# Performance work log

Hardware: AMD Instinct MI355X
Metric: run time of the kernel (lower is better)

## Reference

```python
import jax, jax.numpy as jnp
import numpy as np

B, U1, U2 = 4, 2048, 2048
C = 256      # in_feat_dim
F = 256      # feat_dim
M = 4        # num_modes
D = C // M   # attention_mode_dim = 64
ATTN_CLIP = 500.0
LN_EPS = 1e-12


def setup_inputs() -> dict:
    key = jax.random.key(0)
    ks = jax.random.split(key, 8)
    s = 0.02  # base_initializer_range
    inp = {
        "query_feat": jax.random.normal(ks[0], (B, U1, C), jnp.float32),
        "key_feat": jax.random.normal(ks[1], (B, U2, C), jnp.float32),
        "Wq": jax.random.normal(ks[2], (M * D, C), jnp.float32) * s,
        "bq": jnp.zeros((M * D,), jnp.float32),
    }
    # tie_qk_scheme='shared': key linear shares query weights
    inp["Wk"] = inp["Wq"]
    inp["bk"] = inp["bq"]
    inp["Wv"] = jax.random.normal(ks[3], (M * F, C), jnp.float32) * s  # first_linear, v_has_bias=False
    inp["W_mid"] = jax.random.normal(ks[4], (F, F), jnp.float32) * s   # MMSharedMid shared_linear
    inp["b_mid"] = jnp.zeros((F,), jnp.float32)
    inp["W_out"] = jax.random.normal(ks[5], (M, F, F), jnp.float32) * s  # grouped 1x1 conv, per mode
    inp["b_out"] = jnp.zeros((M, F), jnp.float32)
    inp["ln_g"] = jnp.ones((F,), jnp.float32)   # resout LayerNorm
    inp["ln_b"] = jnp.zeros((F,), jnp.float32)
    inp["W_score"] = jax.random.normal(ks[6], (1, F), jnp.float32) * s  # LearnedSoftAggregate
    inp["b_score"] = jnp.zeros((1,), jnp.float32)
    return inp


def _layer_norm(x, g, b):
    mu = jnp.mean(x, axis=-1, keepdims=True)
    var = jnp.var(x, axis=-1, keepdims=True)
    return (x - mu) * jax.lax.rsqrt(var + LN_EPS) * g + b


def reference(query_feat, key_feat, Wq, bq, Wk, bk, Wv, W_mid, b_mid,
              W_out, b_out, ln_g, ln_b, W_score, b_score):
    # --- tied-QK multi-mode attention ---
    q = (query_feat @ Wq.T + bq).reshape(B, U1, M, D)
    k = (key_feat @ Wk.T + bk).reshape(B, U2, M, D)
    scores = jnp.einsum('bimd,bjmd->bmij', q, k) / jnp.sqrt(jnp.float32(D))
    scores = jnp.clip(scores, -ATTN_CLIP, ATTN_CLIP)  # attn_clip
    probs = jax.nn.softmax(scores, axis=-1)           # [B, M, U1, U2]

    # --- ExpandedFeatTrans: value projection + fusion ---
    v = (key_feat @ Wv.T).reshape(B, U2, M, F)        # first_linear (no bias)
    fused = jnp.einsum('bmij,bjmf->bmif', probs, v)   # [B, M, U1, F]

    # MMSharedMid: shared linear over F + gelu (dropout = identity in eval)
    mid = jax.nn.gelu(fused @ W_mid.T + b_mid, approximate=False)

    # MMPrivateOutput: per-mode grouped 1x1 conv; NOTE the original code computes
    # x_comb = x + shortcut but then layer-norms x (shortcut dropped) - kept faithful.
    out = jnp.einsum('bmif,mgf->bmig', mid, W_out) + b_out[None, :, None, :]
    out = _layer_norm(out, ln_g, ln_b)                # [B, M, U1, F]

    # LearnedSoftAggregate over modes (group_dim=1, keepdim=False)
    mode_scores = out @ W_score.T + b_score           # [B, M, U1, 1]
    mode_probs = jax.nn.softmax(mode_scores, axis=1)
    return jnp.sum(out * mode_probs, axis=1)          # [B, U1, F]
```

## Files before the change

### kernel.cpp

```cpp
#include <hip/hip_runtime.h>

typedef __attribute__((ext_vector_type(8))) short short8;
typedef __attribute__((ext_vector_type(4))) float f32x4;
typedef __attribute__((ext_vector_type(16))) float f32x16;
typedef unsigned short u16t;
typedef unsigned int u32t;

#define MFMA16(a, b, c) __builtin_amdgcn_mfma_f32_16x16x32_bf16((a), (b), (c), 0, 0, 0)
#define MFMA32(a, b, c) __builtin_amdgcn_mfma_f32_32x32x16_bf16((a), (b), (c), 0, 0, 0)

__device__ __forceinline__ u16t f2bf(float f) {
  u32t u = __float_as_uint(f);
  u32t r = u + 0x7fffu + ((u >> 16) & 1u);
  return (u16t)(r >> 16);
}
__device__ __forceinline__ float bf2f(u16t b) {
  return __uint_as_float(((u32t)b) << 16);
}
__device__ __forceinline__ short8 pack8(float4 a0, float4 a1) {
  short8 r;
  r[0] = (short)f2bf(a0.x); r[1] = (short)f2bf(a0.y);
  r[2] = (short)f2bf(a0.z); r[3] = (short)f2bf(a0.w);
  r[4] = (short)f2bf(a1.x); r[5] = (short)f2bf(a1.y);
  r[6] = (short)f2bf(a1.z); r[7] = (short)f2bf(a1.w);
  return r;
}
__device__ __forceinline__ u32t packrhu(float a, float b) {
  u32t ua = __float_as_uint(a) + 0x8000u;
  u32t ub = __float_as_uint(b) + 0x8000u;
  return (ua >> 16) | (ub & 0xffff0000u);
}

__global__ __launch_bounds__(256) void cvt_kernel(
    const float* __restrict__ Wq, const float* __restrict__ Wv,
    const float* __restrict__ Wm, const float* __restrict__ Wo,
    u16t* __restrict__ WqB, u16t* __restrict__ WvB,
    u16t* __restrict__ WmB, u16t* __restrict__ WoB) {
  const int blk = blockIdx.x, tid = threadIdx.x;
  const float* src; u16t* dst; int base;
  if (blk < 64)       { src = Wq; dst = WqB; base = blk * 1024; }
  else if (blk < 320) { src = Wv; dst = WvB; base = (blk - 64) * 1024; }
  else if (blk < 384) { src = Wm; dst = WmB; base = (blk - 320) * 1024; }
  else                { src = Wo; dst = WoB; base = (blk - 384) * 1024; }
  int i = base + tid * 4;
  float4 v = *(const float4*)(src + i);
  ushort4 o;
  o.x = f2bf(v.x); o.y = f2bf(v.y); o.z = f2bf(v.z); o.w = f2bf(v.w);
  *(ushort4*)(dst + i) = o;
}

__global__ __launch_bounds__(256) void proj_kernel(
    const float* __restrict__ query, const float* __restrict__ key,
    const u16t* __restrict__ WqB, const u16t* __restrict__ WvB,
    const float* __restrict__ bq,
    u16t* __restrict__ QfB, u16t* __restrict__ KfB, u16t* __restrict__ VfB) {
  __shared__ __align__(16) u16t As[64 * 264];
  __shared__ __align__(16) u16t Ws[2][64 * 72];

  const int blk = blockIdx.x;
  const int tid = threadIdx.x;
  const int w = tid >> 6, lane = tid & 63, quad = lane >> 4, l15 = lane & 15;
  const int l31 = lane & 31, h8 = (lane >> 5) * 8;
  const int wrow = (w >> 1) * 32, wcol = (w & 1) * 32;
  const int r2 = tid >> 3, c8 = tid & 7;

  const float* A; const u16t* W16; const float* bias;
  float scale; u16t* outp; int mode, bx, by0;
  if (blk < 128) {
    A = query; W16 = WqB; bias = bq; scale = 0.125f; outp = QfB; mode = 0; bx = blk; by0 = 0;
  } else if (blk < 256) {
    A = key; W16 = WqB; bias = bq; scale = 1.0f; outp = KfB; mode = 0; bx = blk - 128; by0 = 0;
  } else {
    int v2 = blk - 256;
    A = key; W16 = WvB; bias = nullptr; scale = 1.0f; outp = VfB; mode = 1;
    bx = v2 & 127; by0 = (v2 >> 7) * 4;
  }
  const int rt = bx * 64;

#pragma unroll
  for (int hh = 0; hh < 2; ++hh) {
    int rr = r2 + hh * 32;
    const float* arow = A + (size_t)(rt + rr) * 256;
#pragma unroll
    for (int kt = 0; kt < 4; ++kt) {
      const float4* pa = (const float4*)(arow + kt * 64 + c8 * 8);
      float4 a0 = pa[0], a1 = pa[1];
      a0.x *= scale; a0.y *= scale; a0.z *= scale; a0.w *= scale;
      a1.x *= scale; a1.y *= scale; a1.z *= scale; a1.w *= scale;
      *(short8*)&As[rr * 264 + kt * 64 + c8 * 8] = pack8(a0, a1);
    }
  }
  __syncthreads();

  short8 af[8][2];
#pragma unroll
  for (int ks8 = 0; ks8 < 8; ++ks8) {
    af[ks8][0] = *(const short8*)&As[(wrow + l15) * 264 + ks8 * 32 + quad * 8];
    af[ks8][1] = *(const short8*)&As[(wrow + 16 + l15) * 264 + ks8 * 32 + quad * 8];
  }

#pragma unroll
  for (int hh = 0; hh < 2; ++hh) {
    int rr = r2 + hh * 32;
    *(short8*)&Ws[0][rr * 72 + c8 * 8] =
        *(const short8*)(W16 + (size_t)(by0 * 64 + rr) * 256 + c8 * 8);
  }
  __syncthreads();

  const f32x4 fz = {0.f, 0.f, 0.f, 0.f};
  f32x4 acc[2][2];
#pragma unroll
  for (int i = 0; i < 2; i++)
#pragma unroll
    for (int j = 0; j < 2; j++) acc[i][j] = fz;

#pragma unroll 1
  for (int nt = 0; nt < 4; ++nt) {
    const int by = by0 + nt;
    const int ct = by * 64;

#pragma unroll
    for (int kt = 0; kt < 4; ++kt) {
      short8 wst[2];
      const bool havenext = (nt < 3) || (kt < 3);
      if (havenext) {
        const int ctn = (kt < 3) ? ct : (ct + 64);
        const int ktn = (kt + 1) & 3;
#pragma unroll
        for (int hh = 0; hh < 2; ++hh) {
          int rr = r2 + hh * 32;
          wst[hh] = *(const short8*)(W16 + (size_t)(ctn + rr) * 256 + ktn * 64 + c8 * 8);
        }
      }
      const u16t* Wb = &Ws[kt & 1][0];
#pragma unroll
      for (int ks = 0; ks < 2; ++ks) {
        short8 bw0 = *(const short8*)&Wb[(wcol + l15) * 72 + ks * 32 + quad * 8];
        short8 bw1 = *(const short8*)&Wb[(wcol + 16 + l15) * 72 + ks * 32 + quad * 8];
        acc[0][0] = MFMA16(af[kt * 2 + ks][0], bw0, acc[0][0]);
        acc[0][1] = MFMA16(af[kt * 2 + ks][0], bw1, acc[0][1]);
        acc[1][0] = MFMA16(af[kt * 2 + ks][1], bw0, acc[1][0]);
        acc[1][1] = MFMA16(af[kt * 2 + ks][1], bw1, acc[1][1]);
      }
      if (havenext) {
#pragma unroll
        for (int hh = 0; hh < 2; ++hh) {
          int rr = r2 + hh * 32;
          *(short8*)&Ws[(kt + 1) & 1][rr * 72 + c8 * 8] = wst[hh];
        }
      }
      __syncthreads();
    }

    u16t* Cs = As;
    if (mode == 0) {
#pragma unroll
      for (int i = 0; i < 2; i++) {
        int rl = wrow + i * 16 + quad * 4;
#pragma unroll
        for (int j = 0; j < 2; j++) {
          int cl = wcol + j * 16 + l15;
          float bv = bias ? bias[ct + cl] * scale : 0.f;
#pragma unroll
          for (int rg = 0; rg < 4; ++rg)
            Cs[(rl + rg) * 72 + cl] = f2bf(acc[i][j][rg] + bv);
        }
      }
    } else {
#pragma unroll
      for (int i = 0; i < 2; i++) {
        int rl = wrow + i * 16 + quad * 4;
#pragma unroll
        for (int j = 0; j < 2; j++) {
          int cl = wcol + j * 16 + l15;
          ushort4 pk;
          pk.x = f2bf(acc[i][j][0]);
          pk.y = f2bf(acc[i][j][1]);
          pk.z = f2bf(acc[i][j][2]);
          pk.w = f2bf(acc[i][j][3]);
          *(ushort4*)&Cs[cl * 72 + rl] = pk;
        }
      }
    }
    __syncthreads();
#pragma unroll
    for (int t2 = 0; t2 < 2; ++t2) {
      short8 frag = *(const short8*)&Cs[(t2 * 32 + l31) * 72 + w * 16 + h8];
      size_t base;
      if (mode == 0) {
        int b = rt >> 11, m = by;
        int it32 = ((rt & 2047) >> 5) + t2;
        base = (((size_t)(b * 4 + m) * 64 + it32) * 4 + w) * 512;
      } else {
        int b = rt >> 11, m = by >> 2;
        int fb = ((by & 3) << 1) + t2;
        int jt16 = ((rt & 2047) >> 4) + w;
        base = (((size_t)(b * 4 + m) * 8 + fb) * 128 + jt16) * 512;
      }
      *(short8*)(outp + base + lane * 8) = frag;
    }
#pragma unroll
    for (int i = 0; i < 2; i++)
#pragma unroll
      for (int j = 0; j < 2; j++) acc[i][j] = fz;
  }
}

__global__ __launch_bounds__(256, 4) void attn_kernel(
    const u16t* __restrict__ Qf, const u16t* __restrict__ Kf,
    const u16t* __restrict__ Vf,
    const u16t* __restrict__ Wmid, const u16t* __restrict__ Wout,
    const float* __restrict__ b_mid, const float* __restrict__ b_out,
    const float* __restrict__ ln_g, const float* __restrict__ ln_b,
    const float* __restrict__ Wsc, const float* __restrict__ b_sc,
    u16t* __restrict__ out_ln, float* __restrict__ scoresWS) {
  __shared__ __align__(16) u16t smU[8448];
  __shared__ float smL[128];
  __shared__ float smR[128];
  __shared__ float smS[64];
  const int tid = threadIdx.x;
  const int w = tid >> 6, lane = tid & 63, quad = lane >> 4, l15 = lane & 15;
  const int l31 = lane & 31, h = lane >> 5;
  const int L = blockIdx.x;
  const int xcd = L & 7, slot = L >> 3;
  const int bm = xcd * 2 + (slot >> 6);
  const int it32 = slot & 63;
  const int m = bm & 3;
  const int q0 = it32 * 32;

  const size_t lane8 = (size_t)lane * 8;

  const u16t* qbase = Qf + ((size_t)(bm * 64 + it32) * 4) * 512 + lane8;
  short8 qf4[4];
#pragma unroll
  for (int ksd = 0; ksd < 4; ++ksd)
    qf4[ksd] = *(const short8*)(qbase + ksd * 512);

  const u16t* kbase = Kf + ((size_t)bm * 256) * 512 + lane8;
  const u16t* vbase = Vf + ((size_t)(bm * 8 + 2 * w) * 128) * 512 + lane8;

  f32x16 facc[2];
#pragma unroll
  for (int j = 0; j < 2; j++)
#pragma unroll
    for (int r = 0; r < 16; r++) facc[j][r] = 0.f;
  float lsum = 0.f;

  short8 kf4[4];
#pragma unroll
  for (int ksd = 0; ksd < 4; ++ksd)
    kf4[ksd] = *(const short8*)(kbase + (size_t)w * 2048 + ksd * 512);

  {
    f32x16 sacc;
#pragma unroll
    for (int r = 0; r < 16; r++) sacc[r] = 0.f;
#pragma unroll
    for (int ksd = 0; ksd < 4; ++ksd)
      sacc = MFMA32(kf4[ksd], qf4[ksd], sacc);
    float ls = 0.f;
#pragma unroll
    for (int tt = 0; tt < 8; ++tt) {
      const int jl = ((2 * tt) & 3) + 8 * ((2 * tt) >> 2) + 4 * h;
      float p0 = __expf(sacc[2 * tt]);
      float p1 = __expf(sacc[2 * tt + 1]);
      ls += p0 + p1;
      *(u32t*)&smU[l31 * 132 + w * 32 + jl] = packrhu(p0, p1);
    }
    lsum += ls;
  }
#pragma unroll
  for (int ksd = 0; ksd < 4; ++ksd)
    kf4[ksd] = *(const short8*)(kbase + (size_t)(4 + w) * 2048 + ksd * 512);
  __syncthreads();

#pragma unroll 1
  for (int t = 0; t < 16; ++t) {
    u16t* Pb = (t & 1) ? smU + 4224 : smU;
    u16t* Pn = (t & 1) ? smU : smU + 4224;

    if (t < 15) {
      f32x16 sacc;
#pragma unroll
      for (int r = 0; r < 16; r++) sacc[r] = 0.f;
#pragma unroll
      for (int ksd = 0; ksd < 4; ++ksd)
        sacc = MFMA32(kf4[ksd], qf4[ksd], sacc);
      float ls = 0.f;
#pragma unroll
      for (int tt = 0; tt < 8; ++tt) {
        const int jl = ((2 * tt) & 3) + 8 * ((2 * tt) >> 2) + 4 * h;
        float p0 = __expf(sacc[2 * tt]);
        float p1 = __expf(sacc[2 * tt + 1]);
        ls += p0 + p1;
        *(u32t*)&Pn[l31 * 132 + w * 32 + jl] = packrhu(p0, p1);
      }
      lsum += ls;
    }
    if (t < 14) {
      const int jn = (t + 2) * 4 + w;
#pragma unroll
      for (int ksd = 0; ksd < 4; ++ksd)
        kf4[ksd] = *(const short8*)(kbase + (size_t)jn * 2048 + ksd * 512);
    }
#pragma unroll
    for (int jj = 0; jj < 4; ++jj) {
      short8 vf[2][2];
#pragma unroll
      for (int fb = 0; fb < 2; ++fb)
#pragma unroll
        for (int ks2 = 0; ks2 < 2; ++ks2)
          vf[fb][ks2] = *(const short8*)(vbase + ((size_t)fb * 128 + (t * 8 + jj * 2 + ks2)) * 512);
      short8 bbL[2];
#pragma unroll
      for (int ks2 = 0; ks2 < 2; ++ks2)
        bbL[ks2] = *(const short8*)&Pb[l31 * 132 + jj * 32 + ks2 * 16 + h * 8];
      facc[0] = MFMA32(vf[0][0], bbL[0], facc[0]);
      facc[0] = MFMA32(vf[0][1], bbL[1], facc[0]);
      facc[1] = MFMA32(vf[1][0], bbL[0], facc[1]);
      facc[1] = MFMA32(vf[1][1], bbL[1], facc[1]);
    }
    __syncthreads();
  }

  lsum += __shfl_xor(lsum, 32);
  if (h == 0) smL[w * 32 + l31] = lsum;
  __syncthreads();
  float inv = 1.f / (smL[l31] + smL[32 + l31] + smL[64 + l31] + smL[96 + l31]);

  u16t* const smF = smU;
#pragma unroll
  for (int fb = 0; fb < 2; ++fb) {
#pragma unroll
    for (int g = 0; g < 4; ++g) {
      int fbase = w * 64 + fb * 32 + 8 * g + 4 * h;
      ushort4 pk4;
      pk4.x = f2bf(facc[fb][4 * g + 0] * inv);
      pk4.y = f2bf(facc[fb][4 * g + 1] * inv);
      pk4.z = f2bf(facc[fb][4 * g + 2] * inv);
      pk4.w = f2bf(facc[fb][4 * g + 3] * inv);
      *(ushort4*)&smF[l31 * 264 + fbase] = pk4;
    }
  }
  __syncthreads();

  const int rgrp = w >> 1, ch = w & 1;
  const int rowq = rgrp * 16 + quad * 4;
  const f32x4 fz4 = {0.f, 0.f, 0.f, 0.f};

  f32x4 macc[8];
#pragma unroll
  for (int i = 0; i < 8; i++) macc[i] = fz4;
  for (int kc = 0; kc < 8; ++kc) {
    short8 af = *(const short8*)&smF[(rgrp * 16 + l15) * 264 + kc * 32 + quad * 8];
#pragma unroll
    for (int nb = 0; nb < 8; ++nb) {
      short8 bw = *(const short8*)(Wmid + (size_t)(ch * 128 + nb * 16 + l15) * 256 + kc * 32 + quad * 8);
      macc[nb] = MFMA16(af, bw, macc[nb]);
    }
  }
#pragma unroll
  for (int nb = 0; nb < 8; ++nb) {
    int c = ch * 128 + nb * 16 + l15;
    float bmv = b_mid[c];
#pragma unroll
    for (int rg = 0; rg < 4; ++rg) {
      float x = macc[nb][rg] + bmv;
      macc[nb][rg] = 0.5f * x * (1.f + erff(x * 0.70710678118654752f));
    }
  }
  __syncthreads();
#pragma unroll
  for (int nb = 0; nb < 8; ++nb)
#pragma unroll
    for (int rg = 0; rg < 4; ++rg)
      smF[(rowq + rg) * 264 + ch * 128 + nb * 16 + l15] = f2bf(macc[nb][rg]);
  __syncthreads();

  const u16t* Wo = Wout + (size_t)m * 65536;
  f32x4 oacc[8];
#pragma unroll
  for (int i = 0; i < 8; i++) oacc[i] = fz4;
  for (int kc = 0; kc < 8; ++kc) {
    short8 af = *(const short8*)&smF[(rgrp * 16 + l15) * 264 + kc * 32 + quad * 8];
#pragma unroll
    for (int nb = 0; nb < 8; ++nb) {
      short8 bw = *(const short8*)(Wo + (size_t)(ch * 128 + nb * 16 + l15) * 256 + kc * 32 + quad * 8);
      oacc[nb] = MFMA16(af, bw, oacc[nb]);
    }
  }

  float sum[4] = {0, 0, 0, 0}, sq[4] = {0, 0, 0, 0};
#pragma unroll
  for (int nb = 0; nb < 8; ++nb) {
    int c = ch * 128 + nb * 16 + l15;
    float bo = b_out[m * 256 + c];
#pragma unroll
    for (int rg = 0; rg < 4; ++rg) {
      float x = oacc[nb][rg] + bo;
      oacc[nb][rg] = x;
      sum[rg] += x;
      sq[rg] += x * x;
    }
  }
#pragma unroll
  for (int rg = 0; rg < 4; ++rg) {
    float s = sum[rg], s2 = sq[rg];
    s += __shfl_xor(s, 1); s += __shfl_xor(s, 2); s += __shfl_xor(s, 4); s += __shfl_xor(s, 8);
    s2 += __shfl_xor(s2, 1); s2 += __shfl_xor(s2, 2); s2 += __shfl_xor(s2, 4); s2 += __shfl_xor(s2, 8);
    if (l15 == 0) {
      smR[(rowq + rg) + 32 * ch] = s;
      smR[64 + (rowq + rg) + 32 * ch] = s2;
    }
  }
  __syncthreads();
  float mu[4], rstd[4];
#pragma unroll
  for (int rg = 0; rg < 4; ++rg) {
    int r = rowq + rg;
    float s = smR[r] + smR[r + 32];
    float s2 = smR[64 + r] + smR[64 + r + 32];
    float mean = s * (1.f / 256.f);
    float var = s2 * (1.f / 256.f) - mean * mean;
    mu[rg] = mean;
    rstd[rg] = rsqrtf(var + 1e-12f);
  }

  float scp[4] = {0, 0, 0, 0};
#pragma unroll
  for (int nb = 0; nb < 8; ++nb) {
    int c = ch * 128 + nb * 16 + l15;
    float g = ln_g[c], bb2 = ln_b[c], wsv = Wsc[c];
#pragma unroll
    for (int rg = 0; rg < 4; ++rg) {
      float xn = (oacc[nb][rg] - mu[rg]) * rstd[rg] * g + bb2;
      out_ln[((size_t)bm * 2048 + (q0 + rowq + rg)) * 256 + c] = f2bf(xn);
      scp[rg] += xn * wsv;
    }
  }
#pragma unroll
  for (int rg = 0; rg < 4; ++rg) {
    float s = scp[rg];
    s += __shfl_xor(s, 1); s += __shfl_xor(s, 2); s += __shfl_xor(s, 4); s += __shfl_xor(s, 8);
    if (l15 == 0) smS[(rowq + rg) + 32 * ch] = s;
  }
  __syncthreads();
  if (ch == 0 && l15 == 0) {
#pragma unroll
    for (int rg = 0; rg < 4; ++rg) {
      int r = rowq + rg;
      scoresWS[bm * 2048 + q0 + r] = smS[r] + smS[r + 32] + b_sc[0];
    }
  }
}

__global__ __launch_bounds__(256) void agg_kernel(
    const u16t* __restrict__ out_ln, const float* __restrict__ scoresWS,
    float* __restrict__ out) {
  const int row = blockIdx.x;
  const int c = threadIdx.x;
  const int b = row >> 11, i = row & 2047;
  float s0 = scoresWS[(b * 4 + 0) * 2048 + i];
  float s1 = scoresWS[(b * 4 + 1) * 2048 + i];
  float s2 = scoresWS[(b * 4 + 2) * 2048 + i];
  float s3 = scoresWS[(b * 4 + 3) * 2048 + i];
  float mx = fmaxf(fmaxf(s0, s1), fmaxf(s2, s3));
  float e0 = __expf(s0 - mx), e1 = __expf(s1 - mx), e2 = __expf(s2 - mx), e3 = __expf(s3 - mx);
  float inv = 1.f / (e0 + e1 + e2 + e3);
  float acc = e0 * inv * bf2f(out_ln[((size_t)(b * 4 + 0) * 2048 + i) * 256 + c]) +
              e1 * inv * bf2f(out_ln[((size_t)(b * 4 + 1) * 2048 + i) * 256 + c]) +
              e2 * inv * bf2f(out_ln[((size_t)(b * 4 + 2) * 2048 + i) * 256 + c]) +
              e3 * inv * bf2f(out_ln[((size_t)(b * 4 + 3) * 2048 + i) * 256 + c]);
  out[(size_t)row * 256 + c] = acc;
}

extern "C" void kernel_launch(void* const* d_in, const int* in_sizes, int n_in,
                              void* d_out, int out_size, void* d_ws, size_t ws_size,
                              hipStream_t stream) {
  (void)in_sizes; (void)n_in; (void)out_size; (void)ws_size;
  const float* query = (const float*)d_in[0];
  const float* key   = (const float*)d_in[1];
  const float* Wq    = (const float*)d_in[2];
  const float* bq    = (const float*)d_in[3];
  const float* Wv    = (const float*)d_in[6];
  const float* Wm    = (const float*)d_in[7];
  const float* bmid  = (const float*)d_in[8];
  const float* Wo    = (const float*)d_in[9];
  const float* bo    = (const float*)d_in[10];
  const float* lng   = (const float*)d_in[11];
  const float* lnb   = (const float*)d_in[12];
  const float* Wsc   = (const float*)d_in[13];
  const float* bsc   = (const float*)d_in[14];

  char* p = (char*)d_ws;
  u16t* QfB = (u16t*)p; p += (size_t)2097152 * 2;
  u16t* KfB = (u16t*)p; p += (size_t)2097152 * 2;
  u16t* VfB = (u16t*)p; p += (size_t)8388608 * 2;
  u16t* WmB = (u16t*)p; p += (size_t)65536 * 2;
  u16t* WoB = (u16t*)p; p += (size_t)262144 * 2;
  u16t* WqB = (u16t*)p; p += (size_t)65536 * 2;
  u16t* WvB = (u16t*)p; p += (size_t)262144 * 2;
  u16t* outLn = (u16t*)p; p += (size_t)8388608 * 2;
  float* scWS = (float*)p; p += (size_t)32768 * 4;

  cvt_kernel<<<640, 256, 0, stream>>>(Wq, Wv, Wm, Wo, WqB, WvB, WmB, WoB);

  proj_kernel<<<768, 256, 0, stream>>>(query, key, WqB, WvB, bq,
                                       QfB, KfB, VfB);

  attn_kernel<<<1024, 256, 0, stream>>>(QfB, KfB, VfB, WmB, WoB,
                                        bmid, bo, lng, lnb, Wsc, bsc,
                                        outLn, scWS);

  agg_kernel<<<8192, 256, 0, stream>>>(outLn, scWS, (float*)d_out);
}
```

Before: 235.0 us.

## Split attention over key halves with atomic fp32 accumulation and separate combine kernel

```diff
diff --git a/kernel.cpp b/kernel.cpp
--- a/kernel.cpp
+++ b/kernel.cpp
@@ -35,8 +35,23 @@
     const float* __restrict__ Wq, const float* __restrict__ Wv,
     const float* __restrict__ Wm, const float* __restrict__ Wo,
     u16t* __restrict__ WqB, u16t* __restrict__ WvB,
-    u16t* __restrict__ WmB, u16t* __restrict__ WoB) {
+    u16t* __restrict__ WmB, u16t* __restrict__ WoB,
+    float* __restrict__ Facc, float* __restrict__ Lsum) {
   const int blk = blockIdx.x, tid = threadIdx.x;
+  if (blk >= 1152) {
+    float* dst = Lsum + (blk - 1152) * 16384 + tid * 4;
+    const float4 z = {0.f, 0.f, 0.f, 0.f};
+#pragma unroll
+    for (int k = 0; k < 16; ++k) *(float4*)(dst + k * 1024) = z;
+    return;
+  }
+  if (blk >= 640) {
+    float* dst = Facc + (size_t)(blk - 640) * 16384 + tid * 4;
+    const float4 z = {0.f, 0.f, 0.f, 0.f};
+#pragma unroll
+    for (int k = 0; k < 16; ++k) *(float4*)(dst + k * 1024) = z;
+    return;
+  }
   const float* src; u16t* dst; int base;
   if (blk < 64)       { src = Wq; dst = WqB; base = blk * 1024; }
   else if (blk < 320) { src = Wv; dst = WvB; base = (blk - 64) * 1024; }
@@ -203,6 +218,290 @@
     for (int i = 0; i < 2; i++)
 #pragma unroll
       for (int j = 0; j < 2; j++) acc[i][j] = fz;
+  }
+}
+
+__global__ __launch_bounds__(256, 4) void attn_part_kernel(
+    const u16t* __restrict__ Qf, const u16t* __restrict__ Kf,
+    const u16t* __restrict__ Vf,
+    float* __restrict__ Facc, float* __restrict__ Lsum) {
+  __shared__ __align__(16) u16t smU[8448];
+  __shared__ float smL[128];
+  const int tid = threadIdx.x;
+  const int w = tid >> 6, lane = tid & 63, l15 = lane & 15;
+  const int l31 = lane & 31, h = lane >> 5;
+  (void)l15;
+  const int L = blockIdx.x;
+  const int xcd = L & 7, slot = L >> 3;
+  const int bm = xcd * 2 + (slot >> 7);
+  const int rest = slot & 127;
+  const int it32 = rest >> 1;
+  const int half = rest & 1;
+  const int t0 = half * 8;
+
+  const size_t lane8 = (size_t)lane * 8;
+
+  const u16t* qbase = Qf + ((size_t)(bm * 64 + it32) * 4) * 512 + lane8;
+  short8 qf4[4];
+#pragma unroll
+  for (int ksd = 0; ksd < 4; ++ksd)
+    qf4[ksd] = *(const short8*)(qbase + ksd * 512);
+
+  const u16t* kbase = Kf + ((size_t)bm * 256) * 512 + lane8;
+  const u16t* vbase = Vf + ((size_t)(bm * 8 + 2 * w) * 128) * 512 + lane8;
+
+  f32x16 facc[2];
+#pragma unroll
+  for (int j = 0; j < 2; j++)
+#pragma unroll
+    for (int r = 0; r < 16; r++) facc[j][r] = 0.f;
+  float lsum = 0.f;
+
+  short8 kf4[4];
+#pragma unroll
+  for (int ksd = 0; ksd < 4; ++ksd)
+    kf4[ksd] = *(const short8*)(kbase + (size_t)(t0 * 4 + w) * 2048 + ksd * 512);
+
+  {
+    f32x16 sacc;
+#pragma unroll
+    for (int r = 0; r < 16; r++) sacc[r] = 0.f;
+#pragma unroll
+    for (int ksd = 0; ksd < 4; ++ksd)
+      sacc = MFMA32(kf4[ksd], qf4[ksd], sacc);
+    float ls = 0.f;
+#pragma unroll
+    for (int tt = 0; tt < 8; ++tt) {
+      const int jl = ((2 * tt) & 3) + 8 * ((2 * tt) >> 2) + 4 * h;
+      float p0 = __expf(sacc[2 * tt]);
+      float p1 = __expf(sacc[2 * tt + 1]);
+      ls += p0 + p1;
+      *(u32t*)&smU[l31 * 132 + w * 32 + jl] = packrhu(p0, p1);
+    }
+    lsum += ls;
+  }
+#pragma unroll
+  for (int ksd = 0; ksd < 4; ++ksd)
+    kf4[ksd] = *(const short8*)(kbase + (size_t)((t0 + 1) * 4 + w) * 2048 + ksd * 512);
+  __syncthreads();
+
+#pragma unroll 1
+  for (int tl = 0; tl < 8; ++tl) {
+    const int t = t0 + tl;
+    u16t* Pb = (tl & 1) ? smU + 4224 : smU;
+    u16t* Pn = (tl & 1) ? smU : smU + 4224;
+
+    if (tl < 7) {
+      f32x16 sacc;
+#pragma unroll
+      for (int r = 0; r < 16; r++) sacc[r] = 0.f;
+#pragma unroll
+      for (int ksd = 0; ksd < 4; ++ksd)
+        sacc = MFMA32(kf4[ksd], qf4[ksd], sacc);
+      float ls = 0.f;
+#pragma unroll
+      for (int tt = 0; tt < 8; ++tt) {
+        const int jl = ((2 * tt) & 3) + 8 * ((2 * tt) >> 2) + 4 * h;
+        float p0 = __expf(sacc[2 * tt]);
+        float p1 = __expf(sacc[2 * tt + 1]);
+        ls += p0 + p1;
+        *(u32t*)&Pn[l31 * 132 + w * 32 + jl] = packrhu(p0, p1);
+      }
+      lsum += ls;
+    }
+    if (tl < 6) {
+      const int jn = (t + 2) * 4 + w;
+#pragma unroll
+      for (int ksd = 0; ksd < 4; ++ksd)
+        kf4[ksd] = *(const short8*)(kbase + (size_t)jn * 2048 + ksd * 512);
+    }
+#pragma unroll
+    for (int jj = 0; jj < 4; ++jj) {
+      short8 vf[2][2];
+#pragma unroll
+      for (int fb = 0; fb < 2; ++fb)
+#pragma unroll
+        for (int ks2 = 0; ks2 < 2; ++ks2)
+          vf[fb][ks2] = *(const short8*)(vbase + ((size_t)fb * 128 + (t * 8 + jj * 2 + ks2)) * 512);
+      short8 bbL[2];
+#pragma unroll
+      for (int ks2 = 0; ks2 < 2; ++ks2)
+        bbL[ks2] = *(const short8*)&Pb[l31 * 132 + jj * 32 + ks2 * 16 + h * 8];
+      facc[0] = MFMA32(vf[0][0], bbL[0], facc[0]);
+      facc[0] = MFMA32(vf[0][1], bbL[1], facc[0]);
+      facc[1] = MFMA32(vf[1][0], bbL[0], facc[1]);
+      facc[1] = MFMA32(vf[1][1], bbL[1], facc[1]);
+    }
+    __syncthreads();
+  }
+
+  lsum += __shfl_xor(lsum, 32);
+  if (h == 0) smL[w * 32 + l31] = lsum;
+  __syncthreads();
+  const size_t tbase = ((size_t)(bm * 64 + it32)) * 32;
+  if (tid < 32) {
+    float lh = smL[tid] + smL[32 + tid] + smL[64 + tid] + smL[96 + tid];
+    atomicAdd(&Lsum[tbase + tid], lh);
+  }
+  float* Fb = Facc + (tbase + l31) * 256;
+#pragma unroll
+  for (int fb = 0; fb < 2; ++fb)
+#pragma unroll
+    for (int g = 0; g < 4; ++g)
+#pragma unroll
+      for (int e = 0; e < 4; ++e) {
+        int f = w * 64 + fb * 32 + 8 * g + 4 * h + e;
+        atomicAdd(&Fb[f], facc[fb][4 * g + e]);
+      }
+}
+
+__global__ __launch_bounds__(256, 4) void combine_kernel(
+    const float* __restrict__ Facc, const float* __restrict__ Lsum,
+    const u16t* __restrict__ Wmid, const u16t* __restrict__ Wout,
+    const float* __restrict__ b_mid, const float* __restrict__ b_out,
+    const float* __restrict__ ln_g, const float* __restrict__ ln_b,
+    const float* __restrict__ Wsc, const float* __restrict__ b_sc,
+    u16t* __restrict__ out_ln, float* __restrict__ scoresWS) {
+  __shared__ __align__(16) u16t smF[8448];
+  __shared__ float smR[128];
+  __shared__ float smS[64];
+  __shared__ float smLi[32];
+  const int tid = threadIdx.x;
+  const int w = tid >> 6, lane = tid & 63, quad = lane >> 4, l15 = lane & 15;
+  const int L = blockIdx.x;
+  const int xcd = L & 7, slot = L >> 3;
+  const int bm = xcd * 2 + (slot >> 6);
+  const int it32 = slot & 63;
+  const int m = bm & 3;
+  const int q0 = it32 * 32;
+
+  const size_t tbase = ((size_t)(bm * 64 + it32)) * 32;
+  if (tid < 32) smLi[tid] = 1.f / Lsum[tbase + tid];
+  __syncthreads();
+
+  const float* Fsrc = Facc + tbase * 256;
+#pragma unroll
+  for (int k = 0; k < 8; ++k) {
+    int flat = (k * 256 + tid) * 4;
+    int row = flat >> 8, f = flat & 255;
+    float4 v = *(const float4*)(Fsrc + flat);
+    float inv = smLi[row];
+    ushort4 pk4;
+    pk4.x = f2bf(v.x * inv);
+    pk4.y = f2bf(v.y * inv);
+    pk4.z = f2bf(v.z * inv);
+    pk4.w = f2bf(v.w * inv);
+    *(ushort4*)&smF[row * 264 + f] = pk4;
+  }
+  __syncthreads();
+
+  const int rgrp = w >> 1, ch = w & 1;
+  const int rowq = rgrp * 16 + quad * 4;
+  const f32x4 fz4 = {0.f, 0.f, 0.f, 0.f};
+
+  f32x4 macc[8];
+#pragma unroll
+  for (int i = 0; i < 8; i++) macc[i] = fz4;
+  for (int kc = 0; kc < 8; ++kc) {
+    short8 af = *(const short8*)&smF[(rgrp * 16 + l15) * 264 + kc * 32 + quad * 8];
+#pragma unroll
+    for (int nb = 0; nb < 8; ++nb) {
+      short8 bw = *(const short8*)(Wmid + (size_t)(ch * 128 + nb * 16 + l15) * 256 + kc * 32 + quad * 8);
+      macc[nb] = MFMA16(af, bw, macc[nb]);
+    }
+  }
+#pragma unroll
+  for (int nb = 0; nb < 8; ++nb) {
+    int c = ch * 128 + nb * 16 + l15;
+    float bmv = b_mid[c];
+#pragma unroll
+    for (int rg = 0; rg < 4; ++rg) {
+      float x = macc[nb][rg] + bmv;
+      macc[nb][rg] = 0.5f * x * (1.f + erff(x * 0.70710678118654752f));
+    }
+  }
+  __syncthreads();
+#pragma unroll
+  for (int nb = 0; nb < 8; ++nb)
+#pragma unroll
+    for (int rg = 0; rg < 4; ++rg)
+      smF[(rowq + rg) * 264 + ch * 128 + nb * 16 + l15] = f2bf(macc[nb][rg]);
+  __syncthreads();
+
+  const u16t* Wo = Wout + (size_t)m * 65536;
+  f32x4 oacc[8];
+#pragma unroll
+  for (int i = 0; i < 8; i++) oacc[i] = fz4;
+  for (int kc = 0; kc < 8; ++kc) {
+    short8 af = *(const short8*)&smF[(rgrp * 16 + l15) * 264 + kc * 32 + quad * 8];
+#pragma unroll
+    for (int nb = 0; nb < 8; ++nb) {
+      short8 bw = *(const short8*)(Wo + (size_t)(ch * 128 + nb * 16 + l15) * 256 + kc * 32 + quad * 8);
+      oacc[nb] = MFMA16(af, bw, oacc[nb]);
+    }
+  }
+
+  float sum[4] = {0, 0, 0, 0}, sq[4] = {0, 0, 0, 0};
+#pragma unroll
+  for (int nb = 0; nb < 8; ++nb) {
+    int c = ch * 128 + nb * 16 + l15;
+    float bo = b_out[m * 256 + c];
+#pragma unroll
+    for (int rg = 0; rg < 4; ++rg) {
+      float x = oacc[nb][rg] + bo;
+      oacc[nb][rg] = x;
+      sum[rg] += x;
+      sq[rg] += x * x;
+    }
+  }
+#pragma unroll
+  for (int rg = 0; rg < 4; ++rg) {
+    float s = sum[rg], s2 = sq[rg];
+    s += __shfl_xor(s, 1); s += __shfl_xor(s, 2); s += __shfl_xor(s, 4); s += __shfl_xor(s, 8);
+    s2 += __shfl_xor(s2, 1); s2 += __shfl_xor(s2, 2); s2 += __shfl_xor(s2, 4); s2 += __shfl_xor(s2, 8);
+    if (l15 == 0) {
+      smR[(rowq + rg) + 32 * ch] = s;
+      smR[64 + (rowq + rg) + 32 * ch] = s2;
+    }
+  }
+  __syncthreads();
+  float mu[4], rstd[4];
+#pragma unroll
+  for (int rg = 0; rg < 4; ++rg) {
+    int r = rowq + rg;
+    float s = smR[r] + smR[r + 32];
+    float s2 = smR[64 + r] + smR[64 + r + 32];
+    float mean = s * (1.f / 256.f);
+    float var = s2 * (1.f / 256.f) - mean * mean;
+    mu[rg] = mean;
+    rstd[rg] = rsqrtf(var + 1e-12f);
+  }
+
+  float scp[4] = {0, 0, 0, 0};
+#pragma unroll
+  for (int nb = 0; nb < 8; ++nb) {
+    int c = ch * 128 + nb * 16 + l15;
+    float g = ln_g[c], bb2 = ln_b[c], wsv = Wsc[c];
+#pragma unroll
+    for (int rg = 0; rg < 4; ++rg) {
+      float xn = (oacc[nb][rg] - mu[rg]) * rstd[rg] * g + bb2;
+      out_ln[((size_t)bm * 2048 + (q0 + rowq + rg)) * 256 + c] = f2bf(xn);
+      scp[rg] += xn * wsv;
+    }
+  }
+#pragma unroll
+  for (int rg = 0; rg < 4; ++rg) {
+    float s = scp[rg];
+    s += __shfl_xor(s, 1); s += __shfl_xor(s, 2); s += __shfl_xor(s, 4); s += __shfl_xor(s, 8);
+    if (l15 == 0) smS[(rowq + rg) + 32 * ch] = s;
+  }
+  __syncthreads();
+  if (ch == 0 && l15 == 0) {
+#pragma unroll
+    for (int rg = 0; rg < 4; ++rg) {
+      int r = rowq + rg;
+      scoresWS[bm * 2048 + q0 + r] = smS[r] + smS[r + 32] + b_sc[0];
+    }
   }
 }
 
@@ -477,7 +776,7 @@
 extern "C" void kernel_launch(void* const* d_in, const int* in_sizes, int n_in,
                               void* d_out, int out_size, void* d_ws, size_t ws_size,
                               hipStream_t stream) {
-  (void)in_sizes; (void)n_in; (void)out_size; (void)ws_size;
+  (void)in_sizes; (void)n_in; (void)out_size;
   const float* query = (const float*)d_in[0];
   const float* key   = (const float*)d_in[1];
   const float* Wq    = (const float*)d_in[2];
@@ -500,17 +799,34 @@
   u16t* WoB = (u16t*)p; p += (size_t)262144 * 2;
   u16t* WqB = (u16t*)p; p += (size_t)65536 * 2;
   u16t* WvB = (u16t*)p; p += (size_t)262144 * 2;
-  u16t* outLn = (u16t*)p; p += (size_t)8388608 * 2;
-  float* scWS = (float*)p; p += (size_t)32768 * 4;
-
-  cvt_kernel<<<640, 256, 0, stream>>>(Wq, Wv, Wm, Wo, WqB, WvB, WmB, WoB);
-
-  proj_kernel<<<768, 256, 0, stream>>>(query, key, WqB, WvB, bq,
-                                       QfB, KfB, VfB);
-
-  attn_kernel<<<1024, 256, 0, stream>>>(QfB, KfB, VfB, WmB, WoB,
-                                        bmid, bo, lng, lnb, Wsc, bsc,
-                                        outLn, scWS);
-
-  agg_kernel<<<8192, 256, 0, stream>>>(outLn, scWS, (float*)d_out);
-}
+  float* Facc = (float*)p;
+  float* Lsum = (float*)(p + (size_t)33554432);
+  float* scWS_s = (float*)(p + (size_t)33554432 + 131072);
+  const size_t need_split = ((char*)scWS_s - (char*)d_ws) + 131072;
+  u16t* outLn_s = (u16t*)d_ws;
+
+  const bool use_split = ws_size >= need_split;
+
+  if (use_split) {
+    cvt_kernel<<<1154, 256, 0, stream>>>(Wq, Wv, Wm, Wo, WqB, WvB, WmB, WoB,
+                                         Facc, Lsum);
+    proj_kernel<<<768, 256, 0, stream>>>(query, key, WqB, WvB, bq,
+                                         QfB, KfB, VfB);
+    attn_part_kernel<<<2048, 256, 0, stream>>>(QfB, KfB, VfB, Facc, Lsum);
+    combine_kernel<<<1024, 256, 0, stream>>>(Facc, Lsum, WmB, WoB,
+                                             bmid, bo, lng, lnb, Wsc, bsc,
+                                             outLn_s, scWS_s);
+    agg_kernel<<<8192, 256, 0, stream>>>(outLn_s, scWS_s, (float*)d_out);
+  } else {
+    u16t* outLn = (u16t*)p; p += (size_t)8388608 * 2;
+    float* scWS = (float*)p; p += (size_t)32768 * 4;
+    cvt_kernel<<<640, 256, 0, stream>>>(Wq, Wv, Wm, Wo, WqB, WvB, WmB, WoB,
+                                        nullptr, nullptr);
+    proj_kernel<<<768, 256, 0, stream>>>(query, key, WqB, WvB, bq,
+                                         QfB, KfB, VfB);
+    attn_kernel<<<1024, 256, 0, stream>>>(QfB, KfB, VfB, WmB, WoB,
+                                          bmid, bo, lng, lnb, Wsc, bsc,
+                                          outLn, scWS);
+    agg_kernel<<<8192, 256, 0, stream>>>(outLn, scWS, (float*)d_out);
+  }
+}
```

Measured after the change: 627.9 us. 167% more time.

## Deepen P-tile shared-memory pipeline to four buffers, one barrier per two tiles

Applied to the files above, without the earlier changes.

```diff
diff --git a/kernel.cpp b/kernel.cpp
--- a/kernel.cpp
+++ b/kernel.cpp
@@ -214,7 +214,7 @@
     const float* __restrict__ ln_g, const float* __restrict__ ln_b,
     const float* __restrict__ Wsc, const float* __restrict__ b_sc,
     u16t* __restrict__ out_ln, float* __restrict__ scoresWS) {
-  __shared__ __align__(16) u16t smU[8448];
+  __shared__ __align__(16) u16t smU[16896];
   __shared__ float smL[128];
   __shared__ float smR[128];
   __shared__ float smS[64];
@@ -251,57 +251,58 @@
   for (int ksd = 0; ksd < 4; ++ksd)
     kf4[ksd] = *(const short8*)(kbase + (size_t)w * 2048 + ksd * 512);
 
-  {
+#pragma unroll
+  for (int pt = 0; pt < 2; ++pt) {
     f32x16 sacc;
 #pragma unroll
     for (int r = 0; r < 16; r++) sacc[r] = 0.f;
 #pragma unroll
     for (int ksd = 0; ksd < 4; ++ksd)
       sacc = MFMA32(kf4[ksd], qf4[ksd], sacc);
+#pragma unroll
+    for (int ksd = 0; ksd < 4; ++ksd)
+      kf4[ksd] = *(const short8*)(kbase + (size_t)((pt + 1) * 4 + w) * 2048 + ksd * 512);
     float ls = 0.f;
+    u16t* Pw = smU + pt * 4224;
 #pragma unroll
     for (int tt = 0; tt < 8; ++tt) {
       const int jl = ((2 * tt) & 3) + 8 * ((2 * tt) >> 2) + 4 * h;
       float p0 = __expf(sacc[2 * tt]);
       float p1 = __expf(sacc[2 * tt + 1]);
       ls += p0 + p1;
-      *(u32t*)&smU[l31 * 132 + w * 32 + jl] = packrhu(p0, p1);
+      *(u32t*)&Pw[l31 * 132 + w * 32 + jl] = packrhu(p0, p1);
     }
     lsum += ls;
   }
-#pragma unroll
-  for (int ksd = 0; ksd < 4; ++ksd)
-    kf4[ksd] = *(const short8*)(kbase + (size_t)(4 + w) * 2048 + ksd * 512);
   __syncthreads();
 
 #pragma unroll 1
-  for (int t = 0; t < 16; ++t) {
-    u16t* Pb = (t & 1) ? smU + 4224 : smU;
-    u16t* Pn = (t & 1) ? smU : smU + 4224;
-
-    if (t < 15) {
+  for (int p = 0; p < 8; ++p) {
+    const int t0 = 2 * p;
+    u16t* Pb0 = smU + ((t0) & 3) * 4224;
+    u16t* Pb1 = smU + ((t0 + 1) & 3) * 4224;
+
+    if (p < 7) {
       f32x16 sacc;
 #pragma unroll
       for (int r = 0; r < 16; r++) sacc[r] = 0.f;
 #pragma unroll
       for (int ksd = 0; ksd < 4; ++ksd)
         sacc = MFMA32(kf4[ksd], qf4[ksd], sacc);
+#pragma unroll
+      for (int ksd = 0; ksd < 4; ++ksd)
+        kf4[ksd] = *(const short8*)(kbase + (size_t)((t0 + 3) * 4 + w) * 2048 + ksd * 512);
       float ls = 0.f;
+      u16t* Pn0 = smU + ((t0 + 2) & 3) * 4224;
 #pragma unroll
       for (int tt = 0; tt < 8; ++tt) {
         const int jl = ((2 * tt) & 3) + 8 * ((2 * tt) >> 2) + 4 * h;
         float p0 = __expf(sacc[2 * tt]);
         float p1 = __expf(sacc[2 * tt + 1]);
         ls += p0 + p1;
-        *(u32t*)&Pn[l31 * 132 + w * 32 + jl] = packrhu(p0, p1);
+        *(u32t*)&Pn0[l31 * 132 + w * 32 + jl] = packrhu(p0, p1);
       }
       lsum += ls;
-    }
-    if (t < 14) {
-      const int jn = (t + 2) * 4 + w;
-#pragma unroll
-      for (int ksd = 0; ksd < 4; ++ksd)
-        kf4[ksd] = *(const short8*)(kbase + (size_t)jn * 2048 + ksd * 512);
     }
 #pragma unroll
     for (int jj = 0; jj < 4; ++jj) {
@@ -310,11 +311,52 @@
       for (int fb = 0; fb < 2; ++fb)
 #pragma unroll
         for (int ks2 = 0; ks2 < 2; ++ks2)
-          vf[fb][ks2] = *(const short8*)(vbase + ((size_t)fb * 128 + (t * 8 + jj * 2 + ks2)) * 512);
+          vf[fb][ks2] = *(const short8*)(vbase + ((size_t)fb * 128 + (t0 * 8 + jj * 2 + ks2)) * 512);
       short8 bbL[2];
 #pragma unroll
       for (int ks2 = 0; ks2 < 2; ++ks2)
-        bbL[ks2] = *(const short8*)&Pb[l31 * 132 + jj * 32 + ks2 * 16 + h * 8];
+        bbL[ks2] = *(const short8*)&Pb0[l31 * 132 + jj * 32 + ks2 * 16 + h * 8];
+      facc[0] = MFMA32(vf[0][0], bbL[0], facc[0]);
+      facc[0] = MFMA32(vf[0][1], bbL[1], facc[0]);
+      facc[1] = MFMA32(vf[1][0], bbL[0], facc[1]);
+      facc[1] = MFMA32(vf[1][1], bbL[1], facc[1]);
+    }
+    if (p < 7) {
+      f32x16 sacc;
+#pragma unroll
+      for (int r = 0; r < 16; r++) sacc[r] = 0.f;
+#pragma unroll
+      for (int ksd = 0; ksd < 4; ++ksd)
+        sacc = MFMA32(kf4[ksd], qf4[ksd], sacc);
+      if (p < 6) {
+#pragma unroll
+        for (int ksd = 0; ksd < 4; ++ksd)
+          kf4[ksd] = *(const short8*)(kbase + (size_t)((t0 + 4) * 4 + w) * 2048 + ksd * 512);
+      }
+      float ls = 0.f;
+      u16t* Pn1 = smU + ((t0 + 3) & 3) * 4224;
+#pragma unroll
+      for (int tt = 0; tt < 8; ++tt) {
+        const int jl = ((2 * tt) & 3) + 8 * ((2 * tt) >> 2) + 4 * h;
+        float p0 = __expf(sacc[2 * tt]);
+        float p1 = __expf(sacc[2 * tt + 1]);
+        ls += p0 + p1;
+        *(u32t*)&Pn1[l31 * 132 + w * 32 + jl] = packrhu(p0, p1);
+      }
+      lsum += ls;
+    }
+#pragma unroll
+    for (int jj = 0; jj < 4; ++jj) {
+      short8 vf[2][2];
+#pragma unroll
+      for (int fb = 0; fb < 2; ++fb)
+#pragma unroll
+        for (int ks2 = 0; ks2 < 2; ++ks2)
+          vf[fb][ks2] = *(const short8*)(vbase + ((size_t)fb * 128 + ((t0 + 1) * 8 + jj * 2 + ks2)) * 512);
+      short8 bbL[2];
+#pragma unroll
+      for (int ks2 = 0; ks2 < 2; ++ks2)
+        bbL[ks2] = *(const short8*)&Pb1[l31 * 132 + jj * 32 + ks2 * 16 + h * 8];
       facc[0] = MFMA32(vf[0][0], bbL[0], facc[0]);
       facc[0] = MFMA32(vf[0][1], bbL[1], facc[0]);
       facc[1] = MFMA32(vf[1][0], bbL[0], facc[1]);
```

Result: no change. 235.9 us (+0.4%).
